# Kernel tuning notes

Hardware: AMD Instinct MI355X
Metric: run time of the kernel (lower is better)

## Reference

```python
import jax, jax.numpy as jnp
import numpy as np

ALPHA = 100.0  # superspike surrogate sharpness (fwd uses hard heaviside)
DT = 0.001
TAU_SYN_INV = 200.0
TAU_MEM_INV = 100.0
V_LEAK = 0.0
V_TH = 1.0
V_RESET = 0.0

@jax.custom_vjp
def heaviside(x):
    return (x > 0).astype(x.dtype)

def _heaviside_fwd(x):
    return heaviside(x), x

def _heaviside_bwd(x, g):
    # norse 'super' (SuperSpike) surrogate gradient
    return (g / (ALPHA * jnp.abs(x) + 1.0) ** 2,)

heaviside.defvjp(_heaviside_fwd, _heaviside_bwd)


def setup_inputs() -> dict:
    key = jax.random.key(0)
    k1, k2 = jax.random.split(key)
    T, B, F = 1024, 128, 512
    input_spikes = jax.random.uniform(k1, (T, B, F), dtype=jnp.float32)
    bound = 1.0 / np.sqrt(F)
    W = jax.random.uniform(k2, (F, F), minval=-bound, maxval=bound, dtype=jnp.float32)
    return {"input_spikes": input_spikes, "W": W}


def reference(input_spikes, W):
    # fc applied per timestep is equivalent to one batched contraction over time
    xs = jnp.einsum('tbf,gf->tbg', input_spikes, W)  # [T,B,F]
    B, F = input_spikes.shape[1], input_spikes.shape[2]

    def step(carry, x_t):
        v, i = carry
        v_decayed = v + DT * TAU_MEM_INV * ((V_LEAK - v) + i)
        i_decayed = i + (-DT * TAU_SYN_INV) * i
        z = heaviside(v_decayed - V_TH)
        v_new = (1.0 - z) * v_decayed + z * V_RESET
        i_new = i_decayed + x_t
        return (v_new, i_new), z

    init = (jnp.zeros((B, F), input_spikes.dtype), jnp.zeros((B, F), input_spikes.dtype))
    (v_final, i_final), zs = jax.lax.scan(step, init, xs)
    z_final = zs[-1]
    # original returns (z, LIFState(z, v, i))
    return z_final, z_final, v_final, i_final
```

## Files before the change

### kernel.cpp

```cpp
#include <hip/hip_runtime.h>


#define T_DIM 1024
#define B_DIM 128
#define F_DIM 512
#define NB (B_DIM * F_DIM)

#define TM 128
#define TN 256
#define KC 32
#define LDA_S 132
#define LDB_S 260

__global__ __launch_bounds__(256, 2)
void gemm_kernel(const float* __restrict__ A, const float* __restrict__ W,
                 float* __restrict__ C) {
    __shared__ float As[KC * LDA_S];
    __shared__ float Bs[KC * LDB_S];
    const int tid = threadIdx.x;
    const int m0 = blockIdx.x * TM;
    const int n0 = blockIdx.y * TN;
    const int tn4 = (tid & 15) * 4;
    const int tm4 = (tid >> 4) * 4;
    const int srow = tid >> 3;
    const int sk = (tid & 7) * 4;

    float acc[8][16];
    #pragma unroll
    for (int i = 0; i < 8; ++i)
        #pragma unroll
        for (int j = 0; j < 16; ++j) acc[i][j] = 0.f;

    for (int k0 = 0; k0 < F_DIM; k0 += KC) {
        float4 av[4], bv[8];
        #pragma unroll
        for (int p = 0; p < 4; ++p)
            av[p] = *(const float4*)(A + (size_t)(m0 + srow + 32 * p) * F_DIM + k0 + sk);
        #pragma unroll
        for (int p = 0; p < 8; ++p)
            bv[p] = *(const float4*)(W + (size_t)(n0 + srow + 32 * p) * F_DIM + k0 + sk);
        __syncthreads();
        #pragma unroll
        for (int p = 0; p < 4; ++p) {
            const int r = srow + 32 * p;
            As[(sk + 0) * LDA_S + r] = av[p].x;  As[(sk + 1) * LDA_S + r] = av[p].y;
            As[(sk + 2) * LDA_S + r] = av[p].z;  As[(sk + 3) * LDA_S + r] = av[p].w;
        }
        #pragma unroll
        for (int p = 0; p < 8; ++p) {
            const int r = srow + 32 * p;
            Bs[(sk + 0) * LDB_S + r] = bv[p].x;  Bs[(sk + 1) * LDB_S + r] = bv[p].y;
            Bs[(sk + 2) * LDB_S + r] = bv[p].z;  Bs[(sk + 3) * LDB_S + r] = bv[p].w;
        }
        __syncthreads();

        #pragma unroll 4
        for (int k = 0; k < KC; ++k) {
            const float4 a0 = *(const float4*)(As + k * LDA_S + tm4);
            const float4 a1 = *(const float4*)(As + k * LDA_S + tm4 + 64);
            const float4 b0 = *(const float4*)(Bs + k * LDB_S + tn4);
            const float4 b1 = *(const float4*)(Bs + k * LDB_S + tn4 + 64);
            const float4 b2 = *(const float4*)(Bs + k * LDB_S + tn4 + 128);
            const float4 b3 = *(const float4*)(Bs + k * LDB_S + tn4 + 192);
            const float a[8] = {a0.x, a0.y, a0.z, a0.w, a1.x, a1.y, a1.z, a1.w};
            const float b[16] = {b0.x, b0.y, b0.z, b0.w, b1.x, b1.y, b1.z, b1.w,
                                 b2.x, b2.y, b2.z, b2.w, b3.x, b3.y, b3.z, b3.w};
            #pragma unroll
            for (int i = 0; i < 8; ++i)
                #pragma unroll
                for (int j = 0; j < 16; ++j)
                    acc[i][j] += a[i] * b[j];
        }
    }

    #pragma unroll
    for (int i = 0; i < 8; ++i) {
        const int m = m0 + ((i < 4) ? (tm4 + i) : (tm4 + 60 + i));
        #pragma unroll
        for (int q = 0; q < 4; ++q) {
            const float4 c = make_float4(acc[i][4 * q + 0], acc[i][4 * q + 1],
                                         acc[i][4 * q + 2], acc[i][4 * q + 3]);
            *(float4*)(C + (size_t)m * F_DIM + n0 + tn4 + 64 * q) = c;
        }
    }
}

#define DEPTH 32

__global__ __launch_bounds__(256)
void scan_kernel(const float* __restrict__ xs, float* __restrict__ vi,
                 float* __restrict__ out, int Tc, int first, int last) {
    const int j = blockIdx.x * 256 + threadIdx.x;
    float v, cur;
    if (first) { v = 0.f; cur = 0.f; }
    else       { v = vi[j]; cur = vi[NB + j]; }
    float z = 0.f;
    const float* pj = xs + j;

    if (Tc >= DEPTH && (Tc % DEPTH) == 0) {
        float buf[DEPTH];
        #pragma unroll
        for (int d = 0; d < DEPTH; ++d) buf[d] = pj[(size_t)d * NB];
        for (int tt = 0; tt < Tc; tt += DEPTH) {
            #pragma unroll
            for (int d = 0; d < DEPTH; ++d) {
                const float x = buf[d];
                int tn = tt + DEPTH + d;
                tn = (tn < Tc) ? tn : 0;
                buf[d] = pj[(size_t)tn * NB];
                const float vd = __fadd_rn(v, __fmul_rn(0.1f, __fsub_rn(cur, v)));
                const float id = __fadd_rn(cur, __fmul_rn(-0.2f, cur));
                const bool sp = vd > 1.0f;
                z = sp ? 1.f : 0.f;
                v = sp ? 0.f : vd;
                cur = __fadd_rn(id, x);
            }
        }
    } else {
        for (int t = 0; t < Tc; ++t) {
            const float x = pj[(size_t)t * NB];
            const float vd = __fadd_rn(v, __fmul_rn(0.1f, __fsub_rn(cur, v)));
            const float id = __fadd_rn(cur, __fmul_rn(-0.2f, cur));
            const bool sp = vd > 1.0f;
            z = sp ? 1.f : 0.f;
            v = sp ? 0.f : vd;
            cur = __fadd_rn(id, x);
        }
    }

    if (last) {
        out[j]           = z;
        out[NB + j]      = z;
        out[2 * NB + j]  = v;
        out[3 * NB + j]  = cur;
    } else {
        vi[j]      = v;
        vi[NB + j] = cur;
    }
}

extern "C" void kernel_launch(void* const* d_in, const int* in_sizes, int n_in,
                              void* d_out, int out_size, void* d_ws, size_t ws_size,
                              hipStream_t stream) {
    const float* S = (const float*)d_in[0];
    const float* W = (const float*)d_in[1];
    float* out = (float*)d_out;
    float* vi = (float*)d_ws;
    float* xs = vi + 2 * NB;
    const size_t avail_f = (ws_size / 4 > (size_t)(2 * NB)) ? ws_size / 4 - 2 * NB : 0;
    int Tc = T_DIM;
    while (Tc > 1 && (size_t)Tc * NB > avail_f) Tc >>= 1;
    const int nc = T_DIM / Tc;
    for (int c = 0; c < nc; ++c) {
        const int M = Tc * B_DIM;
        dim3 grid(M / TM, F_DIM / TN);
        gemm_kernel<<<grid, 256, 0, stream>>>(S + (size_t)c * Tc * NB, W, xs);
        scan_kernel<<<NB / 256, 256, 0, stream>>>(xs, vi, out, Tc,
                                                  (c == 0) ? 1 : 0,
                                                  (c == nc - 1) ? 1 : 0);
    }
}
```

Baseline: 1.043 ms.

## Enlarge GEMM tile to 256x256 with 16x16 microtiles and double-buffered LDS

```diff
diff --git a/kernel.cpp b/kernel.cpp
--- a/kernel.cpp
+++ b/kernel.cpp
@@ -6,76 +6,101 @@
 #define F_DIM 512
 #define NB (B_DIM * F_DIM)
 
-#define TM 128
+#define TM 256
 #define TN 256
-#define KC 32
-#define LDA_S 132
-#define LDB_S 260
+#define KC 8
+#define LDS_ROW 260
+#define T_SZ (KC * LDS_ROW)
 
-__global__ __launch_bounds__(256, 2)
+__global__ __launch_bounds__(256, 1)
 void gemm_kernel(const float* __restrict__ A, const float* __restrict__ W,
                  float* __restrict__ C) {
-    __shared__ float As[KC * LDA_S];
-    __shared__ float Bs[KC * LDB_S];
+    __shared__ float As[2 * T_SZ];
+    __shared__ float Bs[2 * T_SZ];
     const int tid = threadIdx.x;
     const int m0 = blockIdx.x * TM;
     const int n0 = blockIdx.y * TN;
     const int tn4 = (tid & 15) * 4;
-    const int tm4 = (tid >> 4) * 4;
-    const int srow = tid >> 3;
-    const int sk = (tid & 7) * 4;
+    const int tmg = (tid >> 4) * 16;
 
-    float acc[8][16];
+    float acc[16][16];
     #pragma unroll
-    for (int i = 0; i < 8; ++i)
+    for (int i = 0; i < 16; ++i)
         #pragma unroll
         for (int j = 0; j < 16; ++j) acc[i][j] = 0.f;
 
+    const float* arow = A + (size_t)(m0 + tid) * F_DIM;
+    const float* brow = W + (size_t)(n0 + tid) * F_DIM;
+
+    {
+        const float4 a0 = *(const float4*)(arow + 0);
+        const float4 a1 = *(const float4*)(arow + 4);
+        const float4 b0 = *(const float4*)(brow + 0);
+        const float4 b1 = *(const float4*)(brow + 4);
+        As[0 * LDS_ROW + tid] = a0.x;  As[1 * LDS_ROW + tid] = a0.y;
+        As[2 * LDS_ROW + tid] = a0.z;  As[3 * LDS_ROW + tid] = a0.w;
+        As[4 * LDS_ROW + tid] = a1.x;  As[5 * LDS_ROW + tid] = a1.y;
+        As[6 * LDS_ROW + tid] = a1.z;  As[7 * LDS_ROW + tid] = a1.w;
+        Bs[0 * LDS_ROW + tid] = b0.x;  Bs[1 * LDS_ROW + tid] = b0.y;
+        Bs[2 * LDS_ROW + tid] = b0.z;  Bs[3 * LDS_ROW + tid] = b0.w;
+        Bs[4 * LDS_ROW + tid] = b1.x;  Bs[5 * LDS_ROW + tid] = b1.y;
+        Bs[6 * LDS_ROW + tid] = b1.z;  Bs[7 * LDS_ROW + tid] = b1.w;
+        __syncthreads();
+    }
+
+    int cur = 0;
     for (int k0 = 0; k0 < F_DIM; k0 += KC) {
-        float4 av[4], bv[8];
+        const bool more = (k0 + KC < F_DIM);
+        float4 a0, a1, b0, b1;
+        if (more) {
+            a0 = *(const float4*)(arow + k0 + KC);
+            a1 = *(const float4*)(arow + k0 + KC + 4);
+            b0 = *(const float4*)(brow + k0 + KC);
+            b1 = *(const float4*)(brow + k0 + KC + 4);
+        }
+
+        const float* asb = As + cur * T_SZ;
+        const float* bsb = Bs + cur * T_SZ;
         #pragma unroll
-        for (int p = 0; p < 4; ++p)
-            av[p] = *(const float4*)(A + (size_t)(m0 + srow + 32 * p) * F_DIM + k0 + sk);
-        #pragma unroll
-        for (int p = 0; p < 8; ++p)
-            bv[p] = *(const float4*)(W + (size_t)(n0 + srow + 32 * p) * F_DIM + k0 + sk);
-        __syncthreads();
-        #pragma unroll
-        for (int p = 0; p < 4; ++p) {
-            const int r = srow + 32 * p;
-            As[(sk + 0) * LDA_S + r] = av[p].x;  As[(sk + 1) * LDA_S + r] = av[p].y;
-            As[(sk + 2) * LDA_S + r] = av[p].z;  As[(sk + 3) * LDA_S + r] = av[p].w;
-        }
-        #pragma unroll
-        for (int p = 0; p < 8; ++p) {
-            const int r = srow + 32 * p;
-            Bs[(sk + 0) * LDB_S + r] = bv[p].x;  Bs[(sk + 1) * LDB_S + r] = bv[p].y;
-            Bs[(sk + 2) * LDB_S + r] = bv[p].z;  Bs[(sk + 3) * LDB_S + r] = bv[p].w;
-        }
-        __syncthreads();
-
-        #pragma unroll 4
         for (int k = 0; k < KC; ++k) {
-            const float4 a0 = *(const float4*)(As + k * LDA_S + tm4);
-            const float4 a1 = *(const float4*)(As + k * LDA_S + tm4 + 64);
-            const float4 b0 = *(const float4*)(Bs + k * LDB_S + tn4);
-            const float4 b1 = *(const float4*)(Bs + k * LDB_S + tn4 + 64);
-            const float4 b2 = *(const float4*)(Bs + k * LDB_S + tn4 + 128);
-            const float4 b3 = *(const float4*)(Bs + k * LDB_S + tn4 + 192);
-            const float a[8] = {a0.x, a0.y, a0.z, a0.w, a1.x, a1.y, a1.z, a1.w};
-            const float b[16] = {b0.x, b0.y, b0.z, b0.w, b1.x, b1.y, b1.z, b1.w,
-                                 b2.x, b2.y, b2.z, b2.w, b3.x, b3.y, b3.z, b3.w};
+            const float4 av0 = *(const float4*)(asb + k * LDS_ROW + tmg);
+            const float4 av1 = *(const float4*)(asb + k * LDS_ROW + tmg + 4);
+            const float4 av2 = *(const float4*)(asb + k * LDS_ROW + tmg + 8);
+            const float4 av3 = *(const float4*)(asb + k * LDS_ROW + tmg + 12);
+            const float4 bv0 = *(const float4*)(bsb + k * LDS_ROW + tn4);
+            const float4 bv1 = *(const float4*)(bsb + k * LDS_ROW + tn4 + 64);
+            const float4 bv2 = *(const float4*)(bsb + k * LDS_ROW + tn4 + 128);
+            const float4 bv3 = *(const float4*)(bsb + k * LDS_ROW + tn4 + 192);
+            const float a[16] = {av0.x, av0.y, av0.z, av0.w, av1.x, av1.y, av1.z, av1.w,
+                                 av2.x, av2.y, av2.z, av2.w, av3.x, av3.y, av3.z, av3.w};
+            const float b[16] = {bv0.x, bv0.y, bv0.z, bv0.w, bv1.x, bv1.y, bv1.z, bv1.w,
+                                 bv2.x, bv2.y, bv2.z, bv2.w, bv3.x, bv3.y, bv3.z, bv3.w};
             #pragma unroll
-            for (int i = 0; i < 8; ++i)
+            for (int i = 0; i < 16; ++i)
                 #pragma unroll
                 for (int j = 0; j < 16; ++j)
                     acc[i][j] += a[i] * b[j];
         }
+
+        if (more) {
+            float* asn = As + (cur ^ 1) * T_SZ;
+            float* bsn = Bs + (cur ^ 1) * T_SZ;
+            asn[0 * LDS_ROW + tid] = a0.x;  asn[1 * LDS_ROW + tid] = a0.y;
+            asn[2 * LDS_ROW + tid] = a0.z;  asn[3 * LDS_ROW + tid] = a0.w;
+            asn[4 * LDS_ROW + tid] = a1.x;  asn[5 * LDS_ROW + tid] = a1.y;
+            asn[6 * LDS_ROW + tid] = a1.z;  asn[7 * LDS_ROW + tid] = a1.w;
+            bsn[0 * LDS_ROW + tid] = b0.x;  bsn[1 * LDS_ROW + tid] = b0.y;
+            bsn[2 * LDS_ROW + tid] = b0.z;  bsn[3 * LDS_ROW + tid] = b0.w;
+            bsn[4 * LDS_ROW + tid] = b1.x;  bsn[5 * LDS_ROW + tid] = b1.y;
+            bsn[6 * LDS_ROW + tid] = b1.z;  bsn[7 * LDS_ROW + tid] = b1.w;
+            __syncthreads();
+            cur ^= 1;
+        }
     }
 
     #pragma unroll
-    for (int i = 0; i < 8; ++i) {
-        const int m = m0 + ((i < 4) ? (tm4 + i) : (tm4 + 60 + i));
+    for (int i = 0; i < 16; ++i) {
+        const int m = m0 + tmg + i;
         #pragma unroll
         for (int q = 0; q < 4; ++q) {
             const float4 c = make_float4(acc[i][4 * q + 0], acc[i][4 * q + 1],
@@ -149,7 +174,7 @@
     float* xs = vi + 2 * NB;
     const size_t avail_f = (ws_size / 4 > (size_t)(2 * NB)) ? ws_size / 4 - 2 * NB : 0;
     int Tc = T_DIM;
-    while (Tc > 1 && (size_t)Tc * NB > avail_f) Tc >>= 1;
+    while (Tc > 2 && (size_t)Tc * NB > avail_f) Tc >>= 1;
     const int nc = T_DIM / Tc;
     for (int c = 0; c < nc; ++c) {
         const int M = Tc * B_DIM;
```

Measured after the change: 1.747 ms. 67.5% more time.
